# Kernel tuning notes

Hardware: AMD Instinct MI355X
Metric: run time of the kernel (lower is better)

## Reference

```python
import jax, jax.numpy as jnp
import numpy as np

VAR_SCALE = 0.1


def setup_inputs() -> dict:
    key = jax.random.key(0)
    k_x, k_tc, k_task, k_in, k_out = jax.random.split(key, 5)
    B, T, IN, OUT, R = 1024, 8, 4096, 4096, 64
    x = jax.random.normal(k_x, (B, T, IN), dtype=jnp.float32)
    tensor_core = jax.random.normal(k_tc, (R, R, R), dtype=jnp.float32) * VAR_SCALE
    task_core = jax.random.normal(k_task, (T, R), dtype=jnp.float32) * VAR_SCALE
    in_core = jax.random.normal(k_in, (IN, R), dtype=jnp.float32) * VAR_SCALE
    out_core = jax.random.normal(k_out, (OUT, R), dtype=jnp.float32) * VAR_SCALE
    return {"x": x, "tensor_core": tensor_core, "task_core": task_core,
            "in_core": in_core, "out_core": out_core}


def reference(x, tensor_core, task_core, in_core, out_core):
    # Tucker weight reconstruction, faithful to the torch einsum chain.
    # W1: [T, R, R] = task_core @ tensor_core (contract first core mode)
    W = jnp.einsum('tj,jkl->tkl', task_core, tensor_core)
    # W2: [T, IN, R] = contract in_core with middle mode
    W = jnp.einsum('ij,tjk->tik', in_core, W)
    # W3: [T, IN, OUT] = contract out_core with last mode
    W = jnp.einsum('oj,tij->tio', out_core, W)
    # Batched per-task matmul: x [B, T, IN] -> y [B, T, OUT]
    y = jnp.einsum('bti,tio->bto', x, W)
    return y
```

## Files before the change

kernel.cpp:

```cpp
#include <hip/hip_runtime.h>
#include <hip/hip_bf16.h>


typedef __bf16 bf16;
typedef __bf16 bf16x8 __attribute__((ext_vector_type(8)));
typedef __bf16 bf16x4 __attribute__((ext_vector_type(4)));
typedef float  f32x4  __attribute__((ext_vector_type(4)));

__device__ __forceinline__ bf16x8 load_frag_bf16(const bf16* p) {
    return *reinterpret_cast<const bf16x8*>(p);
}

__device__ __forceinline__ bf16x8 load_frag_f32(const float* p) {
    f32x4 a = *reinterpret_cast<const f32x4*>(p);
    f32x4 b = *reinterpret_cast<const f32x4*>(p + 4);
    bf16x8 r;
    r[0] = (bf16)a[0]; r[1] = (bf16)a[1]; r[2] = (bf16)a[2]; r[3] = (bf16)a[3];
    r[4] = (bf16)b[0]; r[5] = (bf16)b[1]; r[6] = (bf16)b[2]; r[7] = (bf16)b[3];
    return r;
}

__device__ __forceinline__ f32x4 mfma16(bf16x8 a, bf16x8 b, f32x4 c) {
    return __builtin_amdgcn_mfma_f32_16x16x32_bf16(a, b, c, 0, 0, 0);
}

__global__ __launch_bounds__(256) void k1_w1t(
    const float* __restrict__ task,
    const float* __restrict__ tensor,
    bf16* __restrict__ w1t)
{
    int t    = blockIdx.x >> 4;
    int part = blockIdx.x & 15;
    int idx  = part * 256 + threadIdx.x;
    int j    = idx >> 6;
    int k    = idx & 63;
    float acc = 0.f;
    #pragma unroll 8
    for (int m = 0; m < 64; ++m)
        acc += task[t * 64 + m] * tensor[(m * 64 + j) * 64 + k];
    w1t[(t * 64 + k) * 64 + j] = (bf16)acc;
}

__global__ __launch_bounds__(256) void k1b_w2t(
    const float* __restrict__ in_core,
    const bf16* __restrict__ w1t,
    bf16* __restrict__ w2t)
{
    int t    = blockIdx.x >> 6;
    int i0   = (blockIdx.x & 63) * 64 + (threadIdx.x >> 6) * 16;
    int lane = threadIdx.x & 63;
    int m    = lane & 15;
    int q    = lane >> 4;

    f32x4 acc[4] = {};
    #pragma unroll
    for (int kc = 0; kc < 64; kc += 32) {
        bf16x8 a = load_frag_f32(in_core + (i0 + m) * 64 + kc + q * 8);
        #pragma unroll
        for (int nt = 0; nt < 4; ++nt) {
            bf16x8 b = load_frag_bf16(w1t + (t * 64 + nt * 16 + m) * 64 + kc + q * 8);
            acc[nt] = mfma16(a, b, acc[nt]);
        }
    }
    #pragma unroll
    for (int nt = 0; nt < 4; ++nt) {
        int n = nt * 16 + m;
        #pragma unroll
        for (int r = 0; r < 4; ++r) {
            int irow = i0 + q * 4 + r;
            w2t[(size_t)(t * 64 + n) * 4096 + irow] = (bf16)acc[nt][r];
        }
    }
}

__global__ __launch_bounds__(256) void k2_p2(
    const float* __restrict__ x,
    const bf16* __restrict__ w2t,
    float* __restrict__ pp,
    int kchunk)
{
    int ks   = blockIdx.x >> 9;
    int rem  = blockIdx.x & 511;
    int t    = rem >> 6;
    int b0   = (rem & 63) * 16;
    int wave = threadIdx.x >> 6;
    int lane = threadIdx.x & 63;
    int m    = lane & 15;
    int q    = lane >> 4;
    int n0   = wave * 16;

    int kbeg = ks * kchunk;
    const float* arow = x   + (size_t)((b0 + m) * 8 + t) * 4096 + kbeg + q * 8;
    const bf16*  brow = w2t + (size_t)(t * 64 + n0 + m) * 4096 + kbeg + q * 8;

    f32x4 acc = {};
    for (int kc = 0; kc < kchunk; kc += 128) {
        bf16x8 a[4], b[4];
        #pragma unroll
        for (int u = 0; u < 4; ++u) {
            a[u] = load_frag_f32(arow + kc + u * 32);
            b[u] = load_frag_bf16(brow + kc + u * 32);
        }
        #pragma unroll
        for (int u = 0; u < 4; ++u)
            acc = mfma16(a[u], b[u], acc);
    }
    float* dst = pp + (size_t)ks * 524288 + (size_t)(t * 1024 + b0) * 64;
    #pragma unroll
    for (int r = 0; r < 4; ++r)
        dst[(q * 4 + r) * 64 + n0 + m] = acc[r];
}

__global__ __launch_bounds__(256) void k_reduce(
    const float* __restrict__ pp,
    bf16* __restrict__ p2,
    int nsplit)
{
    int idx = (blockIdx.x * 256 + threadIdx.x) * 4;
    f32x4 s = *reinterpret_cast<const f32x4*>(pp + idx);
    for (int sp = 1; sp < nsplit; ++sp)
        s += *reinterpret_cast<const f32x4*>(pp + (size_t)sp * 524288 + idx);
    bf16x4 o;
    o[0] = (bf16)s[0]; o[1] = (bf16)s[1]; o[2] = (bf16)s[2]; o[3] = (bf16)s[3];
    *reinterpret_cast<bf16x4*>(p2 + idx) = o;
}

__global__ __launch_bounds__(256) void k4_y(
    const bf16* __restrict__ p2,
    const float* __restrict__ out_core,
    float* __restrict__ y)
{
    int bx    = blockIdx.x;
    int t     = bx >> 8;
    int rest  = bx & 255;
    int mtile = rest >> 5;
    int ntile = rest & 31;
    int wave  = threadIdx.x >> 6;
    int lane  = threadIdx.x & 63;
    int m     = lane & 15;
    int q     = lane >> 4;

    int b_base = mtile * 128 + wave * 32;
    int n_base = ntile * 128;

    f32x4 acc[2][8] = {};
    #pragma unroll
    for (int kc = 0; kc < 64; kc += 32) {
        bf16x8 a0 = load_frag_bf16(p2 + (size_t)(t * 1024 + b_base + m) * 64 + kc + q * 8);
        bf16x8 a1 = load_frag_bf16(p2 + (size_t)(t * 1024 + b_base + 16 + m) * 64 + kc + q * 8);
        #pragma unroll
        for (int nt = 0; nt < 8; ++nt) {
            bf16x8 b = load_frag_f32(out_core + (size_t)(n_base + nt * 16 + m) * 64 + kc + q * 8);
            acc[0][nt] = mfma16(a0, b, acc[0][nt]);
            acc[1][nt] = mfma16(a1, b, acc[1][nt]);
        }
    }
    #pragma unroll
    for (int sub = 0; sub < 2; ++sub) {
        #pragma unroll
        for (int nt = 0; nt < 8; ++nt) {
            int o = n_base + nt * 16 + m;
            #pragma unroll
            for (int r = 0; r < 4; ++r) {
                int b = b_base + sub * 16 + q * 4 + r;
                y[(size_t)(b * 8 + t) * 4096 + o] = acc[sub][nt][r];
            }
        }
    }
}

extern "C" void kernel_launch(void* const* d_in, const int* in_sizes, int n_in,
                              void* d_out, int out_size, void* d_ws, size_t ws_size,
                              hipStream_t stream) {
    const float* x        = (const float*)d_in[0];
    const float* tensor_c = (const float*)d_in[1];
    const float* task_c   = (const float*)d_in[2];
    const float* in_c     = (const float*)d_in[3];
    const float* out_c    = (const float*)d_in[4];
    float* y = (float*)d_out;

    char* ws = (char*)d_ws;
    bf16*  w1t = (bf16*)ws;
    bf16*  w2t = (bf16*)(ws + 65536);
    float* pp  = (float*)(ws + 65536 + (size_t)4 * 1024 * 1024);

    int KS = 4;
    while (KS > 1) {
        size_t need = 65536 + (size_t)4*1024*1024 + (size_t)KS*2097152 + 1048576;
        if (need <= ws_size) break;
        KS >>= 1;
    }
    bf16* p2 = (bf16*)(ws + 65536 + (size_t)4*1024*1024 + (size_t)KS*2097152);
    int kchunk = 4096 / KS;

    k1_w1t  <<<128,      256, 0, stream>>>(task_c, tensor_c, w1t);
    k1b_w2t <<<512,      256, 0, stream>>>(in_c, w1t, w2t);
    k2_p2   <<<512 * KS, 256, 0, stream>>>(x, w2t, pp, kchunk);
    k_reduce<<<512,      256, 0, stream>>>(pp, p2, KS);
    k4_y    <<<2048,     256, 0, stream>>>(p2, out_c, y);
}
```

Baseline: 328.3 us.

## Reassociate Tucker chain: project x by in_core first, fold out_core into task weights

The contraction order changes. x is first projected by in_core, which is shared across tasks, to give z[B*T,64]. The per-task core is then folded with out_core into mt[T,OUT,64], and y = z @ mt^T is computed per task. The x-projection kernel stages x through swizzled LDS with a register prefetch of the next K slab, and the output kernel stages accumulators through LDS so it can write coalesced 16-byte stores. The aim is to stream x once with coalesced row loads instead of strided per-task row access, and to make the y writes coalesced. The cost is an extra transpose kernel and shared-memory barriers.

```diff
diff --git a/kernel.cpp b/kernel.cpp
--- a/kernel.cpp
+++ b/kernel.cpp
@@ -24,10 +24,10 @@
     return __builtin_amdgcn_mfma_f32_16x16x32_bf16(a, b, c, 0, 0, 0);
 }
 
-__global__ __launch_bounds__(256) void k1_w1t(
+__global__ __launch_bounds__(256) void k1_w1(
     const float* __restrict__ task,
     const float* __restrict__ tensor,
-    bf16* __restrict__ w1t)
+    bf16* __restrict__ w1)
 {
     int t    = blockIdx.x >> 4;
     int part = blockIdx.x & 15;
@@ -38,82 +38,119 @@
     #pragma unroll 8
     for (int m = 0; m < 64; ++m)
         acc += task[t * 64 + m] * tensor[(m * 64 + j) * 64 + k];
-    w1t[(t * 64 + k) * 64 + j] = (bf16)acc;
-}
-
-__global__ __launch_bounds__(256) void k1b_w2t(
+    w1[(t * 64 + j) * 64 + k] = (bf16)acc;
+}
+
+__global__ __launch_bounds__(256) void kt_ict(
     const float* __restrict__ in_core,
-    const bf16* __restrict__ w1t,
-    bf16* __restrict__ w2t)
+    bf16* __restrict__ icT)
+{
+    int idx = blockIdx.x * 256 + threadIdx.x;
+    int i0  = (idx & 511) * 8;
+    int j   = idx >> 9;
+    bf16x8 v;
+    #pragma unroll
+    for (int s = 0; s < 8; ++s)
+        v[s] = (bf16)in_core[(size_t)(i0 + s) * 64 + j];
+    *reinterpret_cast<bf16x8*>(icT + (size_t)j * 4096 + i0) = v;
+}
+
+__global__ __launch_bounds__(256) void k2_mt(
+    const float* __restrict__ out_core,
+    const bf16* __restrict__ w1,
+    bf16* __restrict__ mt)
 {
     int t    = blockIdx.x >> 6;
-    int i0   = (blockIdx.x & 63) * 64 + (threadIdx.x >> 6) * 16;
-    int lane = threadIdx.x & 63;
-    int m    = lane & 15;
-    int q    = lane >> 4;
-
-    f32x4 acc[4] = {};
-    #pragma unroll
-    for (int kc = 0; kc < 64; kc += 32) {
-        bf16x8 a = load_frag_f32(in_core + (i0 + m) * 64 + kc + q * 8);
-        #pragma unroll
-        for (int nt = 0; nt < 4; ++nt) {
-            bf16x8 b = load_frag_bf16(w1t + (t * 64 + nt * 16 + m) * 64 + kc + q * 8);
-            acc[nt] = mfma16(a, b, acc[nt]);
-        }
-    }
-    #pragma unroll
-    for (int nt = 0; nt < 4; ++nt) {
-        int n = nt * 16 + m;
-        #pragma unroll
-        for (int r = 0; r < 4; ++r) {
-            int irow = i0 + q * 4 + r;
-            w2t[(size_t)(t * 64 + n) * 4096 + irow] = (bf16)acc[nt][r];
-        }
-    }
-}
-
-__global__ __launch_bounds__(256) void k2_p2(
-    const float* __restrict__ x,
-    const bf16* __restrict__ w2t,
-    float* __restrict__ pp,
-    int kchunk)
-{
-    int ks   = blockIdx.x >> 9;
-    int rem  = blockIdx.x & 511;
-    int t    = rem >> 6;
-    int b0   = (rem & 63) * 16;
+    int ot   = blockIdx.x & 63;
     int wave = threadIdx.x >> 6;
     int lane = threadIdx.x & 63;
     int m    = lane & 15;
     int q    = lane >> 4;
+    int o0   = ot * 64 + wave * 16;
+
+    f32x4 acc[4] = {};
+    #pragma unroll
+    for (int kc = 0; kc < 64; kc += 32) {
+        bf16x8 a = load_frag_f32(out_core + (size_t)(o0 + m) * 64 + kc + q * 8);
+        #pragma unroll
+        for (int nt = 0; nt < 4; ++nt) {
+            bf16x8 b = load_frag_bf16(w1 + (size_t)(t * 64 + nt * 16 + m) * 64 + kc + q * 8);
+            acc[nt] = mfma16(a, b, acc[nt]);
+        }
+    }
+    #pragma unroll
+    for (int nt = 0; nt < 4; ++nt) {
+        #pragma unroll
+        for (int r = 0; r < 4; ++r) {
+            int o = o0 + q * 4 + r;
+            mt[(size_t)(t * 4096 + o) * 64 + nt * 16 + m] = (bf16)acc[nt][r];
+        }
+    }
+}
+
+__global__ __launch_bounds__(256) void k0_z(
+    const float* __restrict__ x,
+    const bf16* __restrict__ icT,
+    float* __restrict__ pp,
+    int kchunk)
+{
+    __shared__ bf16 xs[16 * 256];
+    int ks       = blockIdx.x >> 9;
+    int mt       = blockIdx.x & 511;
+    int row_base = mt * 16;
+    int kbeg     = ks * kchunk;
+    int tid  = threadIdx.x;
+    int r    = tid >> 4;
+    int c16  = tid & 15;
+    int wave = tid >> 6;
+    int lane = tid & 63;
+    int m    = lane & 15;
+    int q    = lane >> 4;
     int n0   = wave * 16;
 
-    int kbeg = ks * kchunk;
-    const float* arow = x   + (size_t)((b0 + m) * 8 + t) * 4096 + kbeg + q * 8;
-    const bf16*  brow = w2t + (size_t)(t * 64 + n0 + m) * 4096 + kbeg + q * 8;
+    const float* gsrc = x   + (size_t)(row_base + r) * 4096 + kbeg;
+    const bf16*  bbas = icT + (size_t)(n0 + m) * 4096 + kbeg;
+
+    f32x4 v[4];
+    #pragma unroll
+    for (int i = 0; i < 4; ++i)
+        v[i] = *reinterpret_cast<const f32x4*>(gsrc + c16 * 4 + i * 64);
 
     f32x4 acc = {};
-    for (int kc = 0; kc < kchunk; kc += 128) {
-        bf16x8 a[4], b[4];
-        #pragma unroll
-        for (int u = 0; u < 4; ++u) {
-            a[u] = load_frag_f32(arow + kc + u * 32);
-            b[u] = load_frag_bf16(brow + kc + u * 32);
-        }
-        #pragma unroll
-        for (int u = 0; u < 4; ++u)
-            acc = mfma16(a[u], b[u], acc);
-    }
-    float* dst = pp + (size_t)ks * 524288 + (size_t)(t * 1024 + b0) * 64;
-    #pragma unroll
-    for (int r = 0; r < 4; ++r)
-        dst[(q * 4 + r) * 64 + n0 + m] = acc[r];
+    for (int kc = 0; kc < kchunk; kc += 256) {
+        __syncthreads();
+        #pragma unroll
+        for (int i = 0; i < 4; ++i) {
+            bf16x4 w;
+            w[0] = (bf16)v[i][0]; w[1] = (bf16)v[i][1];
+            w[2] = (bf16)v[i][2]; w[3] = (bf16)v[i][3];
+            int col = c16 * 4 + i * 64;
+            int u   = (col >> 3) ^ (r & 7);
+            *reinterpret_cast<bf16x4*>(&xs[r * 256 + u * 8 + (col & 7)]) = w;
+        }
+        __syncthreads();
+        if (kc + 256 < kchunk) {
+            #pragma unroll
+            for (int i = 0; i < 4; ++i)
+                v[i] = *reinterpret_cast<const f32x4*>(gsrc + kc + 256 + c16 * 4 + i * 64);
+        }
+        #pragma unroll
+        for (int c = 0; c < 8; ++c) {
+            int u = (c * 4 + q) ^ (m & 7);
+            bf16x8 a = *reinterpret_cast<const bf16x8*>(&xs[m * 256 + u * 8]);
+            bf16x8 b = load_frag_bf16(bbas + kc + c * 32 + q * 8);
+            acc = mfma16(a, b, acc);
+        }
+    }
+    float* dst = pp + (size_t)ks * 524288 + (size_t)row_base * 64;
+    #pragma unroll
+    for (int rr = 0; rr < 4; ++rr)
+        dst[(q * 4 + rr) * 64 + n0 + m] = acc[rr];
 }
 
 __global__ __launch_bounds__(256) void k_reduce(
     const float* __restrict__ pp,
-    bf16* __restrict__ p2,
+    bf16* __restrict__ z,
     int nsplit)
 {
     int idx = (blockIdx.x * 256 + threadIdx.x) * 4;
@@ -122,14 +159,15 @@
         s += *reinterpret_cast<const f32x4*>(pp + (size_t)sp * 524288 + idx);
     bf16x4 o;
     o[0] = (bf16)s[0]; o[1] = (bf16)s[1]; o[2] = (bf16)s[2]; o[3] = (bf16)s[3];
-    *reinterpret_cast<bf16x4*>(p2 + idx) = o;
-}
-
-__global__ __launch_bounds__(256) void k4_y(
-    const bf16* __restrict__ p2,
-    const float* __restrict__ out_core,
+    *reinterpret_cast<bf16x4*>(z + idx) = o;
+}
+
+__global__ __launch_bounds__(256) void k3_y(
+    const bf16* __restrict__ z,
+    const bf16* __restrict__ mt,
     float* __restrict__ y)
 {
+    __shared__ float slab[4 * 2112];
     int bx    = blockIdx.x;
     int t     = bx >> 8;
     int rest  = bx & 255;
@@ -146,26 +184,35 @@
     f32x4 acc[2][8] = {};
     #pragma unroll
     for (int kc = 0; kc < 64; kc += 32) {
-        bf16x8 a0 = load_frag_bf16(p2 + (size_t)(t * 1024 + b_base + m) * 64 + kc + q * 8);
-        bf16x8 a1 = load_frag_bf16(p2 + (size_t)(t * 1024 + b_base + 16 + m) * 64 + kc + q * 8);
+        bf16x8 a0 = load_frag_bf16(z + (size_t)((b_base + m) * 8 + t) * 64 + kc + q * 8);
+        bf16x8 a1 = load_frag_bf16(z + (size_t)((b_base + 16 + m) * 8 + t) * 64 + kc + q * 8);
         #pragma unroll
         for (int nt = 0; nt < 8; ++nt) {
-            bf16x8 b = load_frag_f32(out_core + (size_t)(n_base + nt * 16 + m) * 64 + kc + q * 8);
+            bf16x8 b = load_frag_bf16(mt + (size_t)(t * 4096 + n_base + nt * 16 + m) * 64 + kc + q * 8);
             acc[0][nt] = mfma16(a0, b, acc[0][nt]);
             acc[1][nt] = mfma16(a1, b, acc[1][nt]);
         }
     }
+
+    float* sw = slab + wave * 2112;
     #pragma unroll
     for (int sub = 0; sub < 2; ++sub) {
         #pragma unroll
         for (int nt = 0; nt < 8; ++nt) {
-            int o = n_base + nt * 16 + m;
             #pragma unroll
-            for (int r = 0; r < 4; ++r) {
-                int b = b_base + sub * 16 + q * 4 + r;
-                y[(size_t)(b * 8 + t) * 4096 + o] = acc[sub][nt][r];
-            }
-        }
+            for (int r = 0; r < 4; ++r)
+                sw[(q * 4 + r) * 132 + nt * 16 + m] = acc[sub][nt][r];
+        }
+        __syncthreads();
+        #pragma unroll
+        for (int p = 0; p < 8; ++p) {
+            int row = 2 * p + (lane >> 5);
+            int cu  = lane & 31;
+            f32x4 d = *reinterpret_cast<const f32x4*>(sw + row * 132 + cu * 4);
+            int b   = b_base + sub * 16 + row;
+            *reinterpret_cast<f32x4*>(y + (size_t)(b * 8 + t) * 4096 + n_base + cu * 4) = d;
+        }
+        __syncthreads();
     }
 }
 
@@ -180,22 +227,21 @@
     float* y = (float*)d_out;
 
     char* ws = (char*)d_ws;
-    bf16*  w1t = (bf16*)ws;
-    bf16*  w2t = (bf16*)(ws + 65536);
-    float* pp  = (float*)(ws + 65536 + (size_t)4 * 1024 * 1024);
-
+    bf16*  w1  = (bf16*)ws;
+    bf16*  icT = (bf16*)(ws + (64 << 10));
+    bf16*  mtc = (bf16*)(ws + (64 << 10) + (512 << 10));
+    bf16*  zb  = (bf16*)(ws + (64 << 10) + (512 << 10) + (4 << 20));
+    float* pp  = (float*)(ws + (64 << 10) + (512 << 10) + (4 << 20) + (1 << 20));
+
+    size_t fixed = (size_t)(64 << 10) + (512 << 10) + (4 << 20) + (1 << 20);
     int KS = 4;
-    while (KS > 1) {
-        size_t need = 65536 + (size_t)4*1024*1024 + (size_t)KS*2097152 + 1048576;
-        if (need <= ws_size) break;
-        KS >>= 1;
-    }
-    bf16* p2 = (bf16*)(ws + 65536 + (size_t)4*1024*1024 + (size_t)KS*2097152);
+    while (KS > 1 && fixed + (size_t)KS * 2097152 > ws_size) KS >>= 1;
     int kchunk = 4096 / KS;
 
-    k1_w1t  <<<128,      256, 0, stream>>>(task_c, tensor_c, w1t);
-    k1b_w2t <<<512,      256, 0, stream>>>(in_c, w1t, w2t);
-    k2_p2   <<<512 * KS, 256, 0, stream>>>(x, w2t, pp, kchunk);
-    k_reduce<<<512,      256, 0, stream>>>(pp, p2, KS);
-    k4_y    <<<2048,     256, 0, stream>>>(p2, out_c, y);
-}
+    k1_w1   <<<128,      256, 0, stream>>>(task_c, tensor_c, w1);
+    kt_ict  <<<128,      256, 0, stream>>>(in_c, icT);
+    k2_mt   <<<512,      256, 0, stream>>>(out_c, w1, mtc);
+    k0_z    <<<512 * KS, 256, 0, stream>>>(x, icT, pp, kchunk);
+    k_reduce<<<512,      256, 0, stream>>>(pp, zb, KS);
+    k3_y    <<<2048,     256, 0, stream>>>(zb, mtc, y);
+}
```

New measurement: 285.4 us. -13.1%, faster.
